# Optimization experiments

Hardware: AMD Instinct MI355X
Metric: run time of the kernel (lower is better)

The kernel has to match this reference:

```python
import jax, jax.numpy as jnp
import numpy as np

N, D, T, H, R = 1024, 6, 60, 64, 64
NEG = -10000.0
SLOPE = 0.01  # default LeakyReLU negative slope


def setup_inputs() -> dict:
    key = jax.random.key(0)
    ks = jax.random.split(key, 12)
    x = jax.random.normal(ks[0], (N, D * T), jnp.float32)
    relation_matrix = (jax.random.uniform(ks[1], (N, N, R)) < 0.02).astype(jnp.float32)
    s = 1.0 / np.sqrt(H)
    inp = {
        "x": x,
        "relation_matrix": relation_matrix,
        "W": jax.random.normal(ks[2], (2 * H + R, 1), jnp.float32) / np.sqrt(2 * H + R),
        "b": jnp.zeros((), jnp.float32),
        "fc_w": jax.random.normal(ks[3], (1, 2 * H), jnp.float32) * s,
        "fc_b": jnp.zeros((1,), jnp.float32),
        "Wih0": jax.random.normal(ks[4], (3 * H, D), jnp.float32) * s,
        "Whh0": jax.random.normal(ks[5], (3 * H, H), jnp.float32) * s,
        "bih0": jax.random.normal(ks[6], (3 * H,), jnp.float32) * s,
        "bhh0": jax.random.normal(ks[7], (3 * H,), jnp.float32) * s,
        "Wih1": jax.random.normal(ks[8], (3 * H, H), jnp.float32) * s,
        "Whh1": jax.random.normal(ks[9], (3 * H, H), jnp.float32) * s,
        "bih1": jax.random.normal(ks[10], (3 * H,), jnp.float32) * s,
        "bhh1": jax.random.normal(ks[11], (3 * H,), jnp.float32) * s,
    }
    return inp


def gru_layer(x, Wih, Whh, bih, bhh):
    # x: [N, T, in] -> outputs [N, T, H]; torch GRU gate order: r, z, n
    xg = x @ Wih.T + bih            # [N, T, 3H], input gates precomputed
    xg = jnp.swapaxes(xg, 0, 1)     # [T, N, 3H]

    def step(h, g):
        hg = h @ Whh.T + bhh
        xr, xz, xn = jnp.split(g, 3, axis=-1)
        hr, hz, hn = jnp.split(hg, 3, axis=-1)
        r = jax.nn.sigmoid(xr + hr)
        z = jax.nn.sigmoid(xz + hz)
        n = jnp.tanh(xn + r * hn)
        h = (1.0 - z) * n + z * h
        return h, h

    h0 = jnp.zeros((x.shape[0], Whh.shape[1]), x.dtype)
    _, ys = jax.lax.scan(step, h0, xg)
    return jnp.swapaxes(ys, 0, 1)   # [N, T, H]


def reference(x, relation_matrix, W, b, fc_w, fc_b,
              Wih0, Whh0, bih0, bhh0, Wih1, Whh1, bih1, bhh1):
    # [N, D*T] -> [N, T, D]
    xs = jnp.transpose(x.reshape(x.shape[0], D, -1), (0, 2, 1))
    h = gru_layer(xs, Wih0, Whh0, bih0, bhh0)
    h = gru_layer(h, Wih1, Whh1, bih1, bhh1)
    h = h[:, -1, :]                 # [N, H] last-step hidden

    # score[i,j] = cat(h_i, h_j, rel_ij) @ W + b, computed without the NxNx(2H+R) concat
    Wv = W[:, 0]
    sa = h @ Wv[:H]                              # [N]  (ei part)
    sb = h @ Wv[H:2 * H]                         # [N]  (hidden_batch part)
    sr = jnp.einsum('ijr,r->ij', relation_matrix, Wv[2 * H:])  # [N, N]
    weight = sa[:, None] + sb[None, :] + sr + b
    weight = jnp.where(weight >= 0, weight, SLOPE * weight)    # LeakyReLU

    mask = (relation_matrix.sum(-1) != 0).astype(h.dtype)      # [N, N]
    temp = mask * weight
    temp = jnp.where(temp == 0, NEG, temp)                     # faithful to torch ==0 fill
    valid = jax.nn.softmax(temp, axis=1) * mask

    agg = valid @ h                                            # [N, H]
    hidden = jnp.concatenate([h, agg], axis=1)                 # [N, 2H]
    pred_all = (hidden @ fc_w.T + fc_b).squeeze()
    return pred_all
```

## Files before the change

### kernel.cpp

```cpp
#include <hip/hip_runtime.h>
#include <cstddef>

#define NN 1024
#define DD 6
#define TT 60
#define HH 64
#define NEGV  (-10000.0f)
#define SLOPEV (0.01f)
#define GRUB 64
#define RELB 448

#define PA_RZ 0
#define PA_XN 2432
#define PA_HN 3648
#define PB_RZ 4864
#define PB_XN 7296
#define PB_HN 8512
#define HF0   9728
#define HF1   10944
#define BH0   12160
#define BH1   12736
#define XH    13312
#define SMEMF 17152

typedef _Float16 v8h __attribute__((ext_vector_type(8)));
typedef float    v4f __attribute__((ext_vector_type(4)));

#define MF(a, b, c) __builtin_amdgcn_mfma_f32_16x16x32_f16((a), (b), (c), 0, 0, 0)

__device__ __forceinline__ float sig_(float x)  { return 1.0f / (1.0f + __expf(-x)); }
__device__ __forceinline__ float tanh_(float x) { return 1.0f - 2.0f / (__expf(2.0f * x) + 1.0f); }
__device__ __forceinline__ float bcf_(const float a, const float b) {
    return __builtin_bit_cast(float, __builtin_amdgcn_cvt_pkrtz(a, b));
}
__device__ __forceinline__ v8h zero8() {
    v8h r;
    #pragma unroll
    for (int j = 0; j < 8; ++j) r[j] = (_Float16)0.f;
    return r;
}
__device__ __forceinline__ v8h pack8(const float* __restrict__ p) {
    v8h r;
    #pragma unroll
    for (int j = 0; j < 8; ++j) r[j] = (_Float16)p[j];
    return r;
}
__device__ __forceinline__ v8h pack6(const float* __restrict__ p) {
    v8h r = zero8();
    #pragma unroll
    for (int j = 0; j < 6; ++j) r[j] = (_Float16)p[j];
    return r;
}

__global__ __launch_bounds__(512)
void k_main(const float* __restrict__ x, const float* __restrict__ rel,
            const float* __restrict__ W, const float* __restrict__ fc_w,
            const float* __restrict__ Wih0, const float* __restrict__ Whh0,
            const float* __restrict__ bih0, const float* __restrict__ bhh0,
            const float* __restrict__ Wih1, const float* __restrict__ Whh1,
            const float* __restrict__ bih1, const float* __restrict__ bhh1,
            float* __restrict__ sa, float* __restrict__ sb,
            float* __restrict__ hdot, float* __restrict__ hb,
            float* __restrict__ sr, float* __restrict__ ssum)
{
    __shared__ float smem[SMEMF];
    const int tid = threadIdx.x;

    if (blockIdx.x >= GRUB) {
        const float* __restrict__ Wv = W + 2 * HH;
        const unsigned base = (unsigned)(blockIdx.x - GRUB) * 512 + tid;
        for (unsigned p = base; p < (unsigned)(NN * NN); p += (unsigned)RELB * 512) {
            const float4* b4 = (const float4*)(rel + (size_t)p * 64);
            float4 v[16];
            #pragma unroll
            for (int q = 0; q < 16; ++q) v[q] = b4[q];
            float d0 = 0.f, d1 = 0.f, s0 = 0.f, s1 = 0.f;
            #pragma unroll
            for (int q = 0; q < 16; ++q) {
                d0 += v[q].x * Wv[4*q]   + v[q].z * Wv[4*q+2];
                d1 += v[q].y * Wv[4*q+1] + v[q].w * Wv[4*q+3];
                s0 += v[q].x + v[q].z;
                s1 += v[q].y + v[q].w;
            }
            sr[p]   = d0 + d1;
            ssum[p] = s0 + s1;
        }
        return;
    }

    const int w    = tid >> 6;
    const int lane = tid & 63;
    const int quad = lane >> 4;
    const int mc   = lane & 15;
    const int nb   = blockIdx.x * 16;
    const bool isL0 = (w < 4);
    const int wt   = isL0 ? w : (w - 4);

    for (int idx = tid; idx < TT * 16; idx += 512) {
        const int t = idx >> 4, n = idx & 15;
        const float* xp = x + (size_t)(nb + n) * (DD * TT) + t;
        float4 pk;
        pk.x = bcf_(xp[0],   xp[60]);
        pk.y = bcf_(xp[120], xp[180]);
        pk.z = bcf_(xp[240], xp[300]);
        pk.w = 0.f;
        *(float4*)(smem + XH + idx * 4) = pk;
    }
    for (int idx = tid; idx < 1152; idx += 512) smem[BH0 + idx] = 0.f;
    for (int idx = tid; idx < 2432; idx += 512) smem[HF0 + idx] = 0.f;

    const int r0row = 16 * wt + mc;
    const int zrow  = 64 + 16 * wt + mc;
    const int nrow  = 128 + 16 * wt + mc;
    v8h F0 = zero8(), F1 = zero8(), F2 = zero8(), F3 = zero8();
    v8h F4 = zero8(), F5 = zero8(), F6 = zero8(), F7 = zero8();
    v8h F8 = zero8(), F9 = zero8(), F10 = zero8(), F11 = zero8();
    v8h Xr = zero8(), Xz = zero8(), Xn = zero8();
    if (isL0) {
        F0 = pack8(Whh0 + (size_t)r0row * HH + quad * 8);
        F1 = pack8(Whh0 + (size_t)r0row * HH + 32 + quad * 8);
        F2 = pack8(Whh0 + (size_t)zrow  * HH + quad * 8);
        F3 = pack8(Whh0 + (size_t)zrow  * HH + 32 + quad * 8);
        F4 = pack8(Whh0 + (size_t)nrow  * HH + quad * 8);
        F5 = pack8(Whh0 + (size_t)nrow  * HH + 32 + quad * 8);
        if (quad == 0) {
            Xr = pack6(Wih0 + r0row * DD);
            Xz = pack6(Wih0 + zrow  * DD);
            Xn = pack6(Wih0 + nrow  * DD);
        }
    } else {
        F0 = pack8(Wih1 + (size_t)r0row * HH + quad * 8);
        F1 = pack8(Wih1 + (size_t)r0row * HH + 32 + quad * 8);
        F2 = pack8(Whh1 + (size_t)r0row * HH + quad * 8);
        F3 = pack8(Whh1 + (size_t)r0row * HH + 32 + quad * 8);
        F4 = pack8(Wih1 + (size_t)zrow * HH + quad * 8);
        F5 = pack8(Wih1 + (size_t)zrow * HH + 32 + quad * 8);
        F6 = pack8(Whh1 + (size_t)zrow * HH + quad * 8);
        F7 = pack8(Whh1 + (size_t)zrow * HH + 32 + quad * 8);
        F8 = pack8(Wih1 + (size_t)nrow * HH + quad * 8);
        F9 = pack8(Wih1 + (size_t)nrow * HH + 32 + quad * 8);
        F10 = pack8(Whh1 + (size_t)nrow * HH + quad * 8);
        F11 = pack8(Whh1 + (size_t)nrow * HH + 32 + quad * 8);
    }

    float bR[4], bZ[4], bXn[4], bHn[4];
    #pragma unroll
    for (int e = 0; e < 4; ++e) {
        const int cr = 16 * wt + quad * 4 + e;
        if (isL0) {
            bR[e]  = bih0[cr] + bhh0[cr];
            bZ[e]  = bih0[64 + cr] + bhh0[64 + cr];
            bXn[e] = bih0[128 + cr];
            bHn[e] = bhh0[128 + cr];
        } else {
            bR[e]  = bih1[cr] + bhh1[cr];
            bZ[e]  = bih1[64 + cr] + bhh1[64 + cr];
            bXn[e] = bih1[128 + cr];
            bHn[e] = bhh1[128 + cr];
        }
    }
    __syncthreads();

    auto ldb = [&](int BH, int win) -> v8h {
        return __builtin_bit_cast(v8h,
            *(const float4*)(smem + BH + mc * 36 + win * 16 + quad * 4));
    };
    auto stC = [&](int base, int rowbase, v4f c) {
        #pragma unroll
        for (int e = 0; e < 4; ++e)
            smem[base + (rowbase + quad * 4 + e) * 19 + mc] = c[e];
    };
    auto upd = [&](int PRZ, int PXN, int PHN, int HF, int BH, int lt) {
        const int n = lt & 15, jb = (lt >> 4) * 4;
        float hv[4];
        #pragma unroll
        for (int e = 0; e < 4; ++e) {
            const int j = jb + e;
            const float rp = smem[PRZ + j * 19 + n];
            const float zp = smem[PRZ + (64 + j) * 19 + n];
            const float xn = smem[PXN + j * 19 + n];
            const float hn = smem[PHN + j * 19 + n];
            const float hp = smem[HF + j * 19 + n];
            const float r  = sig_(rp), z = sig_(zp);
            const float nv = tanh_(xn + r * hn);
            const float h  = (1.f - z) * nv + z * hp;
            smem[HF + j * 19 + n] = h;
            hv[e] = h;
        }
        float2 pk;
        pk.x = bcf_(hv[0], hv[1]);
        pk.y = bcf_(hv[2], hv[3]);
        *(float2*)(smem + BH + n * 36 + (jb >> 1)) = pk;
    };

    for (int i = 0; i <= TT; ++i) {
        if (isL0) {
            if (i < TT) {
                const v8h b0 = ldb(BH0, 0);
                const v8h b1 = ldb(BH0, 1);
                const float4 xl = *(const float4*)(smem + XH + (i * 16 + mc) * 4);
                v8h bx = zero8();
                if (quad == 0) bx = __builtin_bit_cast(v8h, xl);

                v4f c = {bR[0], bR[1], bR[2], bR[3]};
                c = MF(F0, b0, c); c = MF(F1, b1, c); c = MF(Xr, bx, c);
                stC(PA_RZ, 16 * wt, c);
                v4f cz = {bZ[0], bZ[1], bZ[2], bZ[3]};
                cz = MF(F2, b0, cz); cz = MF(F3, b1, cz); cz = MF(Xz, bx, cz);
                stC(PA_RZ, 64 + 16 * wt, cz);
                v4f ch = {bHn[0], bHn[1], bHn[2], bHn[3]};
                ch = MF(F4, b0, ch); ch = MF(F5, b1, ch);
                stC(PA_HN, 16 * wt, ch);
                v4f cx = {bXn[0], bXn[1], bXn[2], bXn[3]};
                cx = MF(Xn, bx, cx);
                stC(PA_XN, 16 * wt, cx);
            }
        } else {
            if (i >= 1) {
                const v8h g0 = ldb(BH0, 0);
                const v8h g1 = ldb(BH0, 1);
                const v8h g2 = ldb(BH1, 0);
                const v8h g3 = ldb(BH1, 1);

                v4f c = {bR[0], bR[1], bR[2], bR[3]};
                c = MF(F0, g0, c); c = MF(F1, g1, c); c = MF(F2, g2, c); c = MF(F3, g3, c);
                stC(PB_RZ, 16 * wt, c);
                v4f cz = {bZ[0], bZ[1], bZ[2], bZ[3]};
                cz = MF(F4, g0, cz); cz = MF(F5, g1, cz); cz = MF(F6, g2, cz); cz = MF(F7, g3, cz);
                stC(PB_RZ, 64 + 16 * wt, cz);
                v4f cx = {bXn[0], bXn[1], bXn[2], bXn[3]};
                cx = MF(F8, g0, cx); cx = MF(F9, g1, cx);
                stC(PB_XN, 16 * wt, cx);
                v4f ch = {bHn[0], bHn[1], bHn[2], bHn[3]};
                ch = MF(F10, g2, ch); ch = MF(F11, g3, ch);
                stC(PB_HN, 16 * wt, ch);
            }
        }
        __syncthreads();
        if (tid < 256) {
            if (i < TT) upd(PA_RZ, PA_XN, PA_HN, HF0, BH0, tid);
        } else {
            if (i >= 1) upd(PB_RZ, PB_XN, PB_HN, HF1, BH1, tid - 256);
        }
        __syncthreads();
    }

    if (w < 4) {
        const int n = lane >> 2, p = lane & 3;
        const float* __restrict__ wp = (w == 0) ? W : (w == 1) ? (W + HH)
                                     : (w == 2) ? fc_w : (fc_w + HH);
        float v = 0.f;
        #pragma unroll
        for (int q = 0; q < 16; ++q) {
            const int j = p * 16 + q;
            v += smem[HF1 + j * 19 + n] * wp[j];
        }
        v += __shfl_down(v, 2);
        v += __shfl_down(v, 1);
        if (p == 0) {
            float* dst = (w == 0) ? sa : (w == 1) ? sb : (w == 2) ? hdot : hb;
            dst[nb + n] = v;
        }
    }
}

__global__ __launch_bounds__(256)
void k2(const float* __restrict__ sa, const float* __restrict__ sb,
        const float* __restrict__ hdot, const float* __restrict__ hb,
        const float* __restrict__ sr, const float* __restrict__ ssum,
        const float* __restrict__ bscal, const float* __restrict__ fc_b,
        float* __restrict__ out)
{
    __shared__ float red[12];
    const int i   = blockIdx.x;
    const int tid = threadIdx.x;
    const int j4  = tid * 4;
    const float sai = sa[i] + bscal[0];

    const float4 srv = *(const float4*)(sr   + (size_t)i * NN + j4);
    const float4 ssv = *(const float4*)(ssum + (size_t)i * NN + j4);
    const float4 sbv = *(const float4*)(sb + j4);

    float tv[4], mk[4];
    float mloc = -3.4e38f;
    {
        const float srq[4] = {srv.x, srv.y, srv.z, srv.w};
        const float ssq[4] = {ssv.x, ssv.y, ssv.z, ssv.w};
        const float sbq[4] = {sbv.x, sbv.y, sbv.z, sbv.w};
        #pragma unroll
        for (int q = 0; q < 4; ++q) {
            float wv = sai + sbq[q] + srq[q];
            wv = (wv >= 0.0f) ? wv : SLOPEV * wv;
            const float m = (ssq[q] != 0.0f) ? 1.0f : 0.0f;
            float tt = m * wv;
            tt = (tt == 0.0f) ? NEGV : tt;
            tv[q] = tt; mk[q] = m;
            mloc = fmaxf(mloc, tt);
        }
    }
    #pragma unroll
    for (int off = 32; off >= 1; off >>= 1) mloc = fmaxf(mloc, __shfl_xor(mloc, off));
    if ((tid & 63) == 0) red[tid >> 6] = mloc;
    __syncthreads();
    const float mx = fmaxf(fmaxf(red[0], red[1]), fmaxf(red[2], red[3]));

    const float4 hbv = *(const float4*)(hb + j4);
    const float hbq[4] = {hbv.x, hbv.y, hbv.z, hbv.w};
    float sloc = 0.0f, vloc = 0.0f;
    #pragma unroll
    for (int q = 0; q < 4; ++q) {
        const float e = __expf(tv[q] - mx);
        sloc += e;
        vloc += e * mk[q] * hbq[q];
    }
    #pragma unroll
    for (int off = 32; off >= 1; off >>= 1) {
        sloc += __shfl_xor(sloc, off);
        vloc += __shfl_xor(vloc, off);
    }
    if ((tid & 63) == 0) { red[4 + (tid >> 6)] = sloc; red[8 + (tid >> 6)] = vloc; }
    __syncthreads();
    if (tid == 0) {
        const float denom = red[4] + red[5] + red[6] + red[7];
        const float vsum  = red[8] + red[9] + red[10] + red[11];
        out[i] = hdot[i] + vsum / denom + fc_b[0];
    }
}

extern "C" void kernel_launch(void* const* d_in, const int* in_sizes, int n_in,
                              void* d_out, int out_size, void* d_ws, size_t ws_size,
                              hipStream_t stream)
{
    const float* x     = (const float*)d_in[0];
    const float* rel   = (const float*)d_in[1];
    const float* W     = (const float*)d_in[2];
    const float* b     = (const float*)d_in[3];
    const float* fc_w  = (const float*)d_in[4];
    const float* fc_b  = (const float*)d_in[5];
    const float* Wih0  = (const float*)d_in[6];
    const float* Whh0  = (const float*)d_in[7];
    const float* bih0  = (const float*)d_in[8];
    const float* bhh0  = (const float*)d_in[9];
    const float* Wih1  = (const float*)d_in[10];
    const float* Whh1  = (const float*)d_in[11];
    const float* bih1  = (const float*)d_in[12];
    const float* bhh1  = (const float*)d_in[13];

    float* ws   = (float*)d_ws;
    float* sa   = ws;
    float* sb   = sa   + NN;
    float* hdot = sb   + NN;
    float* hb   = hdot + NN;
    float* sr   = hb   + NN;
    float* ssum = sr   + (size_t)NN * NN;

    k_main<<<GRUB + RELB, 512, 0, stream>>>(x, rel, W, fc_w,
                                            Wih0, Whh0, bih0, bhh0,
                                            Wih1, Whh1, bih1, bhh1,
                                            sa, sb, hdot, hb, sr, ssum);
    k2<<<NN, 256, 0, stream>>>(sa, sb, hdot, hb, sr, ssum,
                               b, fc_b, (float*)d_out);
}
```

Measured before the change: 398.4 us.

## Fuse GRU gate update into MFMA waves with double-buffered hidden state

Each wave now applies the GRU gate nonlinearities directly on its MFMA accumulators and keeps the fp32 hidden state in registers. It no longer stages the gate pre-activations through shared memory for a separate update phase. The packed fp16 hidden state is double-buffered by step parity, which drops one of the two __syncthreads per timestep and shrinks shared memory. The final hidden state is written to LDS once for the output dot products. This relies on the MFMA output lane mapping matching the B-operand packing layout.

```diff
diff --git a/kernel.cpp b/kernel.cpp
--- a/kernel.cpp
+++ b/kernel.cpp
@@ -10,18 +10,11 @@
 #define GRUB 64
 #define RELB 448
 
-#define PA_RZ 0
-#define PA_XN 2432
-#define PA_HN 3648
-#define PB_RZ 4864
-#define PB_XN 7296
-#define PB_HN 8512
-#define HF0   9728
-#define HF1   10944
-#define BH0   12160
-#define BH1   12736
-#define XH    13312
-#define SMEMF 17152
+#define BH0O  0
+#define BH1O  1152
+#define XH    2304
+#define HEP   6144
+#define SMEMF 7232
 
 typedef _Float16 v8h __attribute__((ext_vector_type(8)));
 typedef float    v4f __attribute__((ext_vector_type(4)));
@@ -106,8 +99,7 @@
         pk.w = 0.f;
         *(float4*)(smem + XH + idx * 4) = pk;
     }
-    for (int idx = tid; idx < 1152; idx += 512) smem[BH0 + idx] = 0.f;
-    for (int idx = tid; idx < 2432; idx += 512) smem[HF0 + idx] = 0.f;
+    for (int idx = tid; idx < 2304; idx += 512) smem[idx] = 0.f;
 
     const int r0row = 16 * wt + mc;
     const int zrow  = 64 + 16 * wt + mc;
@@ -159,93 +151,85 @@
             bHn[e] = bhh1[128 + cr];
         }
     }
+
+    float hp[4] = {0.f, 0.f, 0.f, 0.f};
     __syncthreads();
 
-    auto ldb = [&](int BH, int win) -> v8h {
+    auto ldb = [&](const float* basep, int win) -> v8h {
         return __builtin_bit_cast(v8h,
-            *(const float4*)(smem + BH + mc * 36 + win * 16 + quad * 4));
+            *(const float4*)(basep + mc * 36 + win * 16 + quad * 4));
     };
-    auto stC = [&](int base, int rowbase, v4f c) {
-        #pragma unroll
-        for (int e = 0; e < 4; ++e)
-            smem[base + (rowbase + quad * 4 + e) * 19 + mc] = c[e];
+    auto sth = [&](float* basep) {
+        float2 pk;
+        pk.x = bcf_(hp[0], hp[1]);
+        pk.y = bcf_(hp[2], hp[3]);
+        *(float2*)(basep + mc * 36 + 8 * wt + 2 * quad) = pk;
     };
-    auto upd = [&](int PRZ, int PXN, int PHN, int HF, int BH, int lt) {
-        const int n = lt & 15, jb = (lt >> 4) * 4;
-        float hv[4];
+    auto gupd = [&](const v4f& cr, const v4f& cz, const v4f& cx, const v4f& ch) {
         #pragma unroll
         for (int e = 0; e < 4; ++e) {
-            const int j = jb + e;
-            const float rp = smem[PRZ + j * 19 + n];
-            const float zp = smem[PRZ + (64 + j) * 19 + n];
-            const float xn = smem[PXN + j * 19 + n];
-            const float hn = smem[PHN + j * 19 + n];
-            const float hp = smem[HF + j * 19 + n];
-            const float r  = sig_(rp), z = sig_(zp);
-            const float nv = tanh_(xn + r * hn);
-            const float h  = (1.f - z) * nv + z * hp;
-            smem[HF + j * 19 + n] = h;
-            hv[e] = h;
-        }
-        float2 pk;
-        pk.x = bcf_(hv[0], hv[1]);
-        pk.y = bcf_(hv[2], hv[3]);
-        *(float2*)(smem + BH + n * 36 + (jb >> 1)) = pk;
+            const float r  = sig_(cr[e]);
+            const float z  = sig_(cz[e]);
+            const float nv = tanh_(cx[e] + r * ch[e]);
+            hp[e] = (1.f - z) * nv + z * hp[e];
+        }
     };
 
     for (int i = 0; i <= TT; ++i) {
+        const int rbo = (i & 1) * 576;
+        const int wbo = 576 - rbo;
         if (isL0) {
             if (i < TT) {
-                const v8h b0 = ldb(BH0, 0);
-                const v8h b1 = ldb(BH0, 1);
+                const v8h b0 = ldb(smem + BH0O + rbo, 0);
+                const v8h b1 = ldb(smem + BH0O + rbo, 1);
                 const float4 xl = *(const float4*)(smem + XH + (i * 16 + mc) * 4);
                 v8h bx = zero8();
                 if (quad == 0) bx = __builtin_bit_cast(v8h, xl);
 
-                v4f c = {bR[0], bR[1], bR[2], bR[3]};
-                c = MF(F0, b0, c); c = MF(F1, b1, c); c = MF(Xr, bx, c);
-                stC(PA_RZ, 16 * wt, c);
+                v4f cr = {bR[0], bR[1], bR[2], bR[3]};
+                cr = MF(F0, b0, cr); cr = MF(F1, b1, cr); cr = MF(Xr, bx, cr);
                 v4f cz = {bZ[0], bZ[1], bZ[2], bZ[3]};
                 cz = MF(F2, b0, cz); cz = MF(F3, b1, cz); cz = MF(Xz, bx, cz);
-                stC(PA_RZ, 64 + 16 * wt, cz);
                 v4f ch = {bHn[0], bHn[1], bHn[2], bHn[3]};
                 ch = MF(F4, b0, ch); ch = MF(F5, b1, ch);
-                stC(PA_HN, 16 * wt, ch);
                 v4f cx = {bXn[0], bXn[1], bXn[2], bXn[3]};
                 cx = MF(Xn, bx, cx);
-                stC(PA_XN, 16 * wt, cx);
+
+                gupd(cr, cz, cx, ch);
+                sth(smem + BH0O + wbo);
             }
         } else {
             if (i >= 1) {
-                const v8h g0 = ldb(BH0, 0);
-                const v8h g1 = ldb(BH0, 1);
-                const v8h g2 = ldb(BH1, 0);
-                const v8h g3 = ldb(BH1, 1);
-
-                v4f c = {bR[0], bR[1], bR[2], bR[3]};
-                c = MF(F0, g0, c); c = MF(F1, g1, c); c = MF(F2, g2, c); c = MF(F3, g3, c);
-                stC(PB_RZ, 16 * wt, c);
+                const v8h g0 = ldb(smem + BH0O + rbo, 0);
+                const v8h g1 = ldb(smem + BH0O + rbo, 1);
+                const v8h g2 = ldb(smem + BH1O + rbo, 0);
+                const v8h g3 = ldb(smem + BH1O + rbo, 1);
+
+                v4f cr = {bR[0], bR[1], bR[2], bR[3]};
+                cr = MF(F0, g0, cr); cr = MF(F1, g1, cr);
+                cr = MF(F2, g2, cr); cr = MF(F3, g3, cr);
                 v4f cz = {bZ[0], bZ[1], bZ[2], bZ[3]};
-                cz = MF(F4, g0, cz); cz = MF(F5, g1, cz); cz = MF(F6, g2, cz); cz = MF(F7, g3, cz);
-                stC(PB_RZ, 64 + 16 * wt, cz);
+                cz = MF(F4, g0, cz); cz = MF(F5, g1, cz);
+                cz = MF(F6, g2, cz); cz = MF(F7, g3, cz);
                 v4f cx = {bXn[0], bXn[1], bXn[2], bXn[3]};
                 cx = MF(F8, g0, cx); cx = MF(F9, g1, cx);
-                stC(PB_XN, 16 * wt, cx);
                 v4f ch = {bHn[0], bHn[1], bHn[2], bHn[3]};
                 ch = MF(F10, g2, ch); ch = MF(F11, g3, ch);
-                stC(PB_HN, 16 * wt, ch);
+
+                gupd(cr, cz, cx, ch);
+                sth(smem + BH1O + wbo);
             }
         }
         __syncthreads();
-        if (tid < 256) {
-            if (i < TT) upd(PA_RZ, PA_XN, PA_HN, HF0, BH0, tid);
-        } else {
-            if (i >= 1) upd(PB_RZ, PB_XN, PB_HN, HF1, BH1, tid - 256);
-        }
-        __syncthreads();
-    }
-
-    if (w < 4) {
+    }
+
+    if (!isL0) {
+        #pragma unroll
+        for (int e = 0; e < 4; ++e)
+            smem[HEP + (16 * wt + quad * 4 + e) * 17 + mc] = hp[e];
+    }
+    __syncthreads();
+    if (isL0) {
         const int n = lane >> 2, p = lane & 3;
         const float* __restrict__ wp = (w == 0) ? W : (w == 1) ? (W + HH)
                                      : (w == 2) ? fc_w : (fc_w + HH);
@@ -253,7 +237,7 @@
         #pragma unroll
         for (int q = 0; q < 16; ++q) {
             const int j = p * 16 + q;
-            v += smem[HF1 + j * 19 + n] * wp[j];
+            v += smem[HEP + j * 17 + n] * wp[j];
         }
         v += __shfl_down(v, 2);
         v += __shfl_down(v, 1);
```

After: 389.4 us. -2.3%, faster.
